# Kernel optimization log

Hardware: AMD Instinct MI355X
Metric: run time of the kernel (lower is better)

## Reference

```python
import jax, jax.numpy as jnp
import numpy as np
import math

B, L, H, E, D = 4, 2048, 8, 64, 64


def _build_local_log_symmetry_mask(L):
    # Faithful port of LocalLogSymmetryMask: True = masked-out position.
    lws = math.ceil(np.log2(L) / 2)  # local window size
    n_log = math.ceil(10 * np.log2(L))
    m = np.zeros((L, L), dtype=np.float32)
    for i in range(L):
        row = m[i]
        # left side: local window + log-spaced long-range
        if i - lws + 1 < 0:
            row[:i] = 1
        else:
            row[i - lws + 1:i + 1] = 1
            for k in range(n_log):
                ni = i - lws + 1 - int(1.5 ** k)
                if ni >= 0:
                    row[ni] = 1
                else:
                    break
        # right side (symmetric)
        if i + lws - 1 >= L:
            row[i:] = 1
        else:
            row[i:i + lws] = 1
            for k in range(n_log):
                ni = i + lws - 1 + int(1.5 ** k)
                if ni < L:
                    row[ni] = 1
                else:
                    break
    return m == 0  # True where attention is NOT allowed


def setup_inputs() -> dict:
    key = jax.random.key(0)
    kq, kk, kv = jax.random.split(key, 3)
    queries = jax.random.normal(kq, (B, L, H, E), dtype=jnp.float32)
    keys = jax.random.normal(kk, (B, L, H, E), dtype=jnp.float32)
    values = jax.random.normal(kv, (B, L, H, D), dtype=jnp.float32)
    mask = jnp.asarray(_build_local_log_symmetry_mask(L))  # [L, L] bool
    return {"queries": queries, "keys": keys, "values": values, "mask": mask}


def reference(queries, keys, values, mask):
    # queries/keys: [B,L,H,E], values: [B,L,H,D], mask: [L,L] bool (True = masked)
    E_ = queries.shape[-1]
    scale = 1.0 / math.sqrt(E_)
    # scores: [B,H,L,S]
    scores = jnp.einsum("blhe,bshe->bhls", queries, keys) * scale
    scores = jnp.where(mask[None, None, :, :], -jnp.inf, scores)
    attn = jax.nn.softmax(scores, axis=-1)  # dropout disabled (eval mode)
    out = jnp.einsum("bhls,bshd->blhd", attn, values)  # [B,L,H,D]
    return out
```

## Files before the change

### kernel.cpp

```cpp
#include <hip/hip_runtime.h>


#define KB 4
#define KL 2048
#define KH 8
#define KE 64
#define KWAVES 4
#define KROWS (KB * KL * KH)
#define KBLOCKS (KROWS / KWAVES)
#define KROWB (KH * KE * 4)
#define KVROWB 256
#define KWSBYTES ((size_t)KROWS * KVROWB)

typedef __fp16 h2 __attribute__((ext_vector_type(2)));
typedef unsigned ui4 __attribute__((ext_vector_type(4)));

static constexpr int kOff[48] = {
    -5, -4, -3, -2, -1, 0, 1, 2, 3, 4, 5,
    -6, -7, -8, -10, -12, -16, -22, -30, -43, -62, -91, -134, -199, -296,
    -442, -661, -990, -1482,
    6, 7, 8, 10, 12, 16, 22, 30, 43, 62, 91, 134, 199, 296, 442, 661, 990,
    1482,
    1 << 19};

template <int CTRL>
__device__ __forceinline__ float dpp_radd(float x) {
    int t = __builtin_amdgcn_update_dpp(0, __float_as_int(x), CTRL, 0xF, 0xF,
                                        false);
    return x + __int_as_float(t);
}
template <int CTRL>
__device__ __forceinline__ unsigned dpp_mov_u(unsigned x) {
    return (unsigned)__builtin_amdgcn_update_dpp(0, (int)x, CTRL, 0xF, 0xF,
                                                 false);
}

#if __has_builtin(__builtin_amdgcn_permlane16_swap)
__device__ __forceinline__ void pl16(float x, float& a, float& b) {
    auto r = __builtin_amdgcn_permlane16_swap(__float_as_uint(x),
                                              __float_as_uint(x), false, false);
    a = __uint_as_float(r[0]);
    b = __uint_as_float(r[1]);
}
#else
__device__ __forceinline__ void pl16(float x, float& a, float& b) {
    a = x;
    b = __shfl_xor(x, 16, 64);
}
#endif
#if __has_builtin(__builtin_amdgcn_permlane32_swap)
__device__ __forceinline__ void pl32(float x, float& a, float& b) {
    auto r = __builtin_amdgcn_permlane32_swap(__float_as_uint(x),
                                              __float_as_uint(x), false, false);
    a = __uint_as_float(r[0]);
    b = __uint_as_float(r[1]);
}
#else
__device__ __forceinline__ void pl32(float x, float& a, float& b) {
    a = x;
    b = __shfl_xor(x, 32, 64);
}
#endif
__device__ __forceinline__ float red16_add(float x) {
    float a, b;
    pl16(x, a, b);
    return a + b;
}
__device__ __forceinline__ float red32_add(float x) {
    float a, b;
    pl32(x, a, b);
    return a + b;
}

#if __has_builtin(__builtin_amdgcn_exp2f)
#define KEXP2(x) __builtin_amdgcn_exp2f(x)
#else
#define KEXP2(x) exp2f(x)
#endif

__device__ __forceinline__ h2 pkrtz(float a, float b) {
#if __has_builtin(__builtin_amdgcn_cvt_pkrtz)
    return __builtin_amdgcn_cvt_pkrtz(a, b);
#else
    h2 r;
    r[0] = (__fp16)a;
    r[1] = (__fp16)b;
    return r;
#endif
}
__device__ __forceinline__ float fd2(h2 a, h2 b, float c) {
#if __has_builtin(__builtin_amdgcn_fdot2)
    return __builtin_amdgcn_fdot2(a, b, c, false);
#else
    return fmaf((float)a[1], (float)b[1], fmaf((float)a[0], (float)b[0], c));
#endif
}
__device__ __forceinline__ h2 as_h2(unsigned u) {
    return __builtin_bit_cast(h2, u);
}

__global__ __launch_bounds__(256) void MaskAttention_prep_kernel(
    const float* __restrict__ k, const float* __restrict__ v,
    unsigned* __restrict__ kv) {
    const unsigned t  = (unsigned)blockIdx.x * 256u + (unsigned)threadIdx.x;
    const unsigned qd = t & 15u;
    const unsigned gr = t >> 4;
    const unsigned j  = gr & (KL - 1);
    const unsigned bh = gr >> 11;
    const unsigned b  = bh >> 3;
    const unsigned h  = bh & 7;
    const unsigned m  = qd >> 1;
    const float* __restrict__ src = (qd & 1u) ? v : k;
    const float* s =
        src + ((((size_t)b * KL + j) * KH + h) * KE + (size_t)m * 8);
    const float4 x = *(const float4*)s;
    const float4 y = *(const float4*)(s + 4);
    ui4 o;
    o[0] = __builtin_bit_cast(unsigned, pkrtz(x.x, x.y));
    o[1] = __builtin_bit_cast(unsigned, pkrtz(x.z, x.w));
    o[2] = __builtin_bit_cast(unsigned, pkrtz(y.x, y.y));
    o[3] = __builtin_bit_cast(unsigned, pkrtz(y.z, y.w));
    *(ui4*)((char*)kv + (size_t)gr * KVROWB + (size_t)qd * 16) = o;
}

__global__ __launch_bounds__(256) void MaskAttention_20572893347881_kernel(
    const float* __restrict__ q, const unsigned* __restrict__ kv,
    float* __restrict__ out) {
    const int tid  = (int)threadIdx.x;
    const int lane = tid & 63;
    const int g    = lane >> 4;
    const int e4   = lane & 15;
    const int wave = __builtin_amdgcn_readfirstlane(tid >> 6);

    const int p = (int)blockIdx.x;
    const int l = (p & 7) * (KBLOCKS / 8) + (p >> 3);
    const int r = l * KWAVES + wave;
    const int i  = r & (KL - 1);
    const int bh = r >> 11;

    const char* __restrict__ kvb =
        (const char*)kv + (size_t)bh * (KL * KVROWB);
    const size_t hbB = (size_t)(bh >> 3) * (KL * KROWB) +
                       (size_t)(bh & 7) * (KE * 4);
    const char* __restrict__ qc = (const char*)q + hbB;
    char* __restrict__ oc       = (char*)out + hbB;

    const unsigned co     = (unsigned)(e4 * 16);
    const unsigned base_r = (unsigned)i * KVROWB + co;
    const unsigned clampv = (unsigned)(KL - 1) * KVROWB + co;

    const bool g1 = (g & 1) != 0;
    const bool g2 = (g & 2) != 0;

    unsigned off[12];
    bool ok[12];
#pragma unroll
    for (int t = 0; t < 12; ++t) {
        const int a0 = kOff[4 * t + 0] * KVROWB;
        const int a1 = kOff[4 * t + 1] * KVROWB;
        const int a2 = kOff[4 * t + 2] * KVROWB;
        const int a3 = kOff[4 * t + 3] * KVROWB;
        const int dd = g1 ? (g2 ? a3 : a1) : (g2 ? a2 : a0);
        const unsigned u = base_r + (unsigned)dd;
        ok[t]  = u < (unsigned)(KL * KVROWB);
        off[t] = u < clampv ? u : clampv;
    }

    const float4 qf = *(const float4*)(qc + (unsigned)i * KROWB + co);
    const float qs  = 0.125f * 1.44269504088896340736f;
    const h2 qa = pkrtz(qf.x * qs, qf.y * qs);
    const h2 qb = pkrtz(qf.z * qs, qf.w * qs);
    const h2 qan =
        as_h2(dpp_mov_u<0x101>(__builtin_bit_cast(unsigned, qa)));
    const h2 qbn =
        as_h2(dpp_mov_u<0x101>(__builtin_bit_cast(unsigned, qb)));

    float dsum = 0.f;
    float a0 = 0.f, a1 = 0.f, a2 = 0.f, a3 = 0.f;
    float a4 = 0.f, a5 = 0.f, a6 = 0.f, a7 = 0.f;
#pragma unroll
    for (int t = 0; t < 12; ++t) {
        const ui4 w = *(const ui4*)(kvb + off[t]);
        float sd = fd2(as_h2(w[0]), qa,
                       fd2(as_h2(w[1]), qb,
                           fd2(as_h2(w[2]), qan, fd2(as_h2(w[3]), qbn, 0.f))));
        sd = dpp_radd<0x122>(sd);
        sd = dpp_radd<0x124>(sd);
        sd = dpp_radd<0x128>(sd);
        const float pp = ok[t] ? KEXP2(sd) : 0.f;
        const float pv =
            __uint_as_float(dpp_mov_u<0x111>(__float_as_uint(pp)));
        dsum += pv;
        const h2 v01 = as_h2(w[0]), v23 = as_h2(w[1]);
        const h2 v45 = as_h2(w[2]), v67 = as_h2(w[3]);
        a0 = fmaf(pv, (float)v01[0], a0);
        a1 = fmaf(pv, (float)v01[1], a1);
        a2 = fmaf(pv, (float)v23[0], a2);
        a3 = fmaf(pv, (float)v23[1], a3);
        a4 = fmaf(pv, (float)v45[0], a4);
        a5 = fmaf(pv, (float)v45[1], a5);
        a6 = fmaf(pv, (float)v67[0], a6);
        a7 = fmaf(pv, (float)v67[1], a7);
    }

    float d = red32_add(red16_add(dsum));
    const float inv = __builtin_amdgcn_rcpf(d);
    a0 = red32_add(red16_add(a0));
    a1 = red32_add(red16_add(a1));
    a2 = red32_add(red16_add(a2));
    a3 = red32_add(red16_add(a3));
    a4 = red32_add(red16_add(a4));
    a5 = red32_add(red16_add(a5));
    a6 = red32_add(red16_add(a6));
    a7 = red32_add(red16_add(a7));

    if ((lane < 16) && (lane & 1)) {
        const int m = lane >> 1;
        char* dst = oc + (unsigned)i * KROWB + (unsigned)m * 32;
        float4 o0 = make_float4(a0 * inv, a1 * inv, a2 * inv, a3 * inv);
        float4 o1 = make_float4(a4 * inv, a5 * inv, a6 * inv, a7 * inv);
        *(float4*)dst = o0;
        *(float4*)(dst + 16) = o1;
    }
}

__global__ __launch_bounds__(256) void MaskAttention_f32_fallback_kernel(
    const float* __restrict__ q, const float* __restrict__ k,
    const float* __restrict__ v, float* __restrict__ out) {
    const int tid  = (int)threadIdx.x;
    const int lane = tid & 63;
    const int g    = lane >> 4;
    const int e4   = lane & 15;
    const int wave = __builtin_amdgcn_readfirstlane(tid >> 6);
    const int p = (int)blockIdx.x;
    const int l = (p & 7) * (KBLOCKS / 8) + (p >> 3);
    const int r = l * KWAVES + wave;
    const int i = r & (KL - 1);
    const int h = (r >> 11) & (KH - 1);
    const int b = r >> 14;
    const size_t hbB = (size_t)b * (KL * KROWB) + (size_t)h * (KE * 4);
    const char* __restrict__ qc = (const char*)q + hbB;
    const char* __restrict__ kc = (const char*)k + hbB;
    const char* __restrict__ vc = (const char*)v + hbB;
    char* __restrict__ oc       = (char*)out + hbB;
    const unsigned co     = (unsigned)(e4 * 16);
    const unsigned base   = (unsigned)i * KROWB + co;
    const unsigned clampv = (unsigned)((KL - 1) * KROWB) + co;
    const bool g1 = (g & 1) != 0;
    const bool g2 = (g & 2) != 0;
    unsigned off[12];
    bool ok[12];
#pragma unroll
    for (int t = 0; t < 12; ++t) {
        const int a0 = kOff[4 * t + 0] * KROWB;
        const int a1 = kOff[4 * t + 1] * KROWB;
        const int a2 = kOff[4 * t + 2] * KROWB;
        const int a3 = kOff[4 * t + 3] * KROWB;
        const int dd = g1 ? (g2 ? a3 : a1) : (g2 ? a2 : a0);
        const unsigned u = base + (unsigned)dd;
        ok[t]  = u < (unsigned)(KL * KROWB);
        off[t] = u < clampv ? u : clampv;
    }
    float4 qf = *(const float4*)(qc + base);
    const float qs = 0.125f * 1.44269504088896340736f;
    qf.x *= qs; qf.y *= qs; qf.z *= qs; qf.w *= qs;
    float dsum = 0.f;
    float4 acc = make_float4(0.f, 0.f, 0.f, 0.f);
#pragma unroll
    for (int t = 0; t < 12; ++t) {
        const float4 kf = *(const float4*)(kc + off[t]);
        const float4 vf = *(const float4*)(vc + off[t]);
        float sd = qf.x * kf.x + qf.y * kf.y + qf.z * kf.z + qf.w * kf.w;
        sd = dpp_radd<0x121>(sd);
        sd = dpp_radd<0x122>(sd);
        sd = dpp_radd<0x124>(sd);
        sd = dpp_radd<0x128>(sd);
        const float pr = ok[t] ? KEXP2(sd) : 0.f;
        dsum += pr;
        acc.x = fmaf(pr, vf.x, acc.x);
        acc.y = fmaf(pr, vf.y, acc.y);
        acc.z = fmaf(pr, vf.z, acc.z);
        acc.w = fmaf(pr, vf.w, acc.w);
    }
    float d = red32_add(red16_add(dsum));
    const float inv = __builtin_amdgcn_rcpf(d);
    acc.x = red32_add(red16_add(acc.x));
    acc.y = red32_add(red16_add(acc.y));
    acc.z = red32_add(red16_add(acc.z));
    acc.w = red32_add(red16_add(acc.w));
    if (lane < 16) {
        float4 o = make_float4(acc.x * inv, acc.y * inv, acc.z * inv,
                               acc.w * inv);
        *(float4*)(oc + base) = o;
    }
}

extern "C" void kernel_launch(void* const* d_in, const int* in_sizes, int n_in,
                              void* d_out, int out_size, void* d_ws,
                              size_t ws_size, hipStream_t stream) {
    (void)in_sizes; (void)n_in; (void)out_size;
    const float* q = (const float*)d_in[0];
    const float* k = (const float*)d_in[1];
    const float* v = (const float*)d_in[2];
    float* out = (float*)d_out;

    if (d_ws != nullptr && ws_size >= KWSBYTES) {
        unsigned* kv = (unsigned*)d_ws;
        hipLaunchKernelGGL(MaskAttention_prep_kernel,
                           dim3(KROWS * 16 / 256), dim3(256), 0, stream,
                           k, v, kv);
        hipLaunchKernelGGL(MaskAttention_20572893347881_kernel,
                           dim3(KBLOCKS), dim3(KWAVES * 64), 0, stream,
                           q, kv, out);
    } else {
        hipLaunchKernelGGL(MaskAttention_f32_fallback_kernel,
                           dim3(KBLOCKS), dim3(KWAVES * 64), 0, stream,
                           q, k, v, out);
    }
}
```

Measured before the change: 142.9 us.

## Accumulate PV in packed fp16 FMA, table offsets in LDS, merge prep loads

Replaces the eight fp32 FMAs per key with four packed-half FMAs and does the cross-lane reductions on packed halves. Per-lane offset selection moves to a small LDS table, which adds a block barrier. The prep kernel now has each thread convert both the K and V slices, halving its grid, and the DPP move uses bound_ctrl. The aim is to cut ALU instruction count, at the risk of lower accumulation precision with fp16 sums.

```diff
diff --git a/kernel.cpp b/kernel.cpp
--- a/kernel.cpp
+++ b/kernel.cpp
@@ -30,46 +30,72 @@
     return x + __int_as_float(t);
 }
 template <int CTRL>
+__device__ __forceinline__ unsigned dpp_mov1_u(unsigned x) {
+#if __has_builtin(__builtin_amdgcn_mov_dpp)
+    return (unsigned)__builtin_amdgcn_mov_dpp((int)x, CTRL, 0xF, 0xF, true);
+#else
+    return (unsigned)__builtin_amdgcn_update_dpp(0, (int)x, CTRL, 0xF, 0xF,
+                                                 true);
+#endif
+}
+template <int CTRL>
 __device__ __forceinline__ unsigned dpp_mov_u(unsigned x) {
     return (unsigned)__builtin_amdgcn_update_dpp(0, (int)x, CTRL, 0xF, 0xF,
                                                  false);
 }
 
 #if __has_builtin(__builtin_amdgcn_permlane16_swap)
-__device__ __forceinline__ void pl16(float x, float& a, float& b) {
-    auto r = __builtin_amdgcn_permlane16_swap(__float_as_uint(x),
-                                              __float_as_uint(x), false, false);
-    a = __uint_as_float(r[0]);
-    b = __uint_as_float(r[1]);
-}
-#else
-__device__ __forceinline__ void pl16(float x, float& a, float& b) {
+#define KHAVE_PL16 1
+__device__ __forceinline__ void pl16u(unsigned x, unsigned& a, unsigned& b) {
+    auto r = __builtin_amdgcn_permlane16_swap(x, x, false, false);
+    a = r[0];
+    b = r[1];
+}
+#else
+#define KHAVE_PL16 0
+__device__ __forceinline__ void pl16u(unsigned x, unsigned& a, unsigned& b) {
     a = x;
-    b = __shfl_xor(x, 16, 64);
+    b = (unsigned)__shfl_xor((int)x, 16, 64);
 }
 #endif
 #if __has_builtin(__builtin_amdgcn_permlane32_swap)
-__device__ __forceinline__ void pl32(float x, float& a, float& b) {
-    auto r = __builtin_amdgcn_permlane32_swap(__float_as_uint(x),
-                                              __float_as_uint(x), false, false);
-    a = __uint_as_float(r[0]);
-    b = __uint_as_float(r[1]);
-}
-#else
-__device__ __forceinline__ void pl32(float x, float& a, float& b) {
+__device__ __forceinline__ void pl32u(unsigned x, unsigned& a, unsigned& b) {
+    auto r = __builtin_amdgcn_permlane32_swap(x, x, false, false);
+    a = r[0];
+    b = r[1];
+}
+#else
+__device__ __forceinline__ void pl32u(unsigned x, unsigned& a, unsigned& b) {
     a = x;
-    b = __shfl_xor(x, 32, 64);
-}
-#endif
+    b = (unsigned)__shfl_xor((int)x, 32, 64);
+}
+#endif
+
 __device__ __forceinline__ float red16_add(float x) {
-    float a, b;
-    pl16(x, a, b);
-    return a + b;
+    unsigned a, b;
+    pl16u(__float_as_uint(x), a, b);
+    return __uint_as_float(a) + __uint_as_float(b);
 }
 __device__ __forceinline__ float red32_add(float x) {
-    float a, b;
-    pl32(x, a, b);
-    return a + b;
+    unsigned a, b;
+    pl32u(__float_as_uint(x), a, b);
+    return __uint_as_float(a) + __uint_as_float(b);
+}
+__device__ __forceinline__ h2 as_h2(unsigned u) {
+    return __builtin_bit_cast(h2, u);
+}
+__device__ __forceinline__ unsigned as_u(h2 x) {
+    return __builtin_bit_cast(unsigned, x);
+}
+__device__ __forceinline__ h2 red16_pk(h2 x) {
+    unsigned a, b;
+    pl16u(as_u(x), a, b);
+    return as_h2(a) + as_h2(b);
+}
+__device__ __forceinline__ h2 red32_pk(h2 x) {
+    unsigned a, b;
+    pl32u(as_u(x), a, b);
+    return as_h2(a) + as_h2(b);
 }
 
 #if __has_builtin(__builtin_amdgcn_exp2f)
@@ -95,32 +121,36 @@
     return fmaf((float)a[1], (float)b[1], fmaf((float)a[0], (float)b[0], c));
 #endif
 }
-__device__ __forceinline__ h2 as_h2(unsigned u) {
-    return __builtin_bit_cast(h2, u);
-}
 
 __global__ __launch_bounds__(256) void MaskAttention_prep_kernel(
     const float* __restrict__ k, const float* __restrict__ v,
     unsigned* __restrict__ kv) {
     const unsigned t  = (unsigned)blockIdx.x * 256u + (unsigned)threadIdx.x;
-    const unsigned qd = t & 15u;
-    const unsigned gr = t >> 4;
+    const unsigned m  = t & 7u;
+    const unsigned gr = t >> 3;
     const unsigned j  = gr & (KL - 1);
     const unsigned bh = gr >> 11;
     const unsigned b  = bh >> 3;
     const unsigned h  = bh & 7;
-    const unsigned m  = qd >> 1;
-    const float* __restrict__ src = (qd & 1u) ? v : k;
-    const float* s =
-        src + ((((size_t)b * KL + j) * KH + h) * KE + (size_t)m * 8);
-    const float4 x = *(const float4*)s;
-    const float4 y = *(const float4*)(s + 4);
-    ui4 o;
-    o[0] = __builtin_bit_cast(unsigned, pkrtz(x.x, x.y));
-    o[1] = __builtin_bit_cast(unsigned, pkrtz(x.z, x.w));
-    o[2] = __builtin_bit_cast(unsigned, pkrtz(y.x, y.y));
-    o[3] = __builtin_bit_cast(unsigned, pkrtz(y.z, y.w));
-    *(ui4*)((char*)kv + (size_t)gr * KVROWB + (size_t)qd * 16) = o;
+    const size_t el = (((size_t)b * KL + j) * KH + h) * KE + (size_t)m * 8;
+    const float* sk = k + el;
+    const float* sv = v + el;
+    const float4 kx = *(const float4*)sk;
+    const float4 ky = *(const float4*)(sk + 4);
+    const float4 vx = *(const float4*)sv;
+    const float4 vy = *(const float4*)(sv + 4);
+    ui4 ok_, ov_;
+    ok_[0] = as_u(pkrtz(kx.x, kx.y));
+    ok_[1] = as_u(pkrtz(kx.z, kx.w));
+    ok_[2] = as_u(pkrtz(ky.x, ky.y));
+    ok_[3] = as_u(pkrtz(ky.z, ky.w));
+    ov_[0] = as_u(pkrtz(vx.x, vx.y));
+    ov_[1] = as_u(pkrtz(vx.z, vx.w));
+    ov_[2] = as_u(pkrtz(vy.x, vy.y));
+    ov_[3] = as_u(pkrtz(vy.z, vy.w));
+    char* dst = (char*)kv + (size_t)gr * KVROWB + (size_t)m * 32;
+    *(ui4*)dst        = ok_;
+    *(ui4*)(dst + 16) = ov_;
 }
 
 __global__ __launch_bounds__(256) void MaskAttention_20572893347881_kernel(
@@ -132,6 +162,10 @@
     const int e4   = lane & 15;
     const int wave = __builtin_amdgcn_readfirstlane(tid >> 6);
 
+    __shared__ int ddt[48];
+    if (tid < 48) ddt[tid] = kOff[tid] * KVROWB;
+    __syncthreads();
+
     const int p = (int)blockIdx.x;
     const int l = (p & 7) * (KBLOCKS / 8) + (p >> 3);
     const int r = l * KWAVES + wave;
@@ -149,19 +183,11 @@
     const unsigned base_r = (unsigned)i * KVROWB + co;
     const unsigned clampv = (unsigned)(KL - 1) * KVROWB + co;
 
-    const bool g1 = (g & 1) != 0;
-    const bool g2 = (g & 2) != 0;
-
     unsigned off[12];
     bool ok[12];
 #pragma unroll
     for (int t = 0; t < 12; ++t) {
-        const int a0 = kOff[4 * t + 0] * KVROWB;
-        const int a1 = kOff[4 * t + 1] * KVROWB;
-        const int a2 = kOff[4 * t + 2] * KVROWB;
-        const int a3 = kOff[4 * t + 3] * KVROWB;
-        const int dd = g1 ? (g2 ? a3 : a1) : (g2 ? a2 : a0);
-        const unsigned u = base_r + (unsigned)dd;
+        const unsigned u = base_r + (unsigned)ddt[4 * t + g];
         ok[t]  = u < (unsigned)(KL * KVROWB);
         off[t] = u < clampv ? u : clampv;
     }
@@ -170,14 +196,11 @@
     const float qs  = 0.125f * 1.44269504088896340736f;
     const h2 qa = pkrtz(qf.x * qs, qf.y * qs);
     const h2 qb = pkrtz(qf.z * qs, qf.w * qs);
-    const h2 qan =
-        as_h2(dpp_mov_u<0x101>(__builtin_bit_cast(unsigned, qa)));
-    const h2 qbn =
-        as_h2(dpp_mov_u<0x101>(__builtin_bit_cast(unsigned, qb)));
+    const h2 qan = as_h2(dpp_mov_u<0x101>(as_u(qa)));
+    const h2 qbn = as_h2(dpp_mov_u<0x101>(as_u(qb)));
 
     float dsum = 0.f;
-    float a0 = 0.f, a1 = 0.f, a2 = 0.f, a3 = 0.f;
-    float a4 = 0.f, a5 = 0.f, a6 = 0.f, a7 = 0.f;
+    h2 acc01 = {0, 0}, acc23 = {0, 0}, acc45 = {0, 0}, acc67 = {0, 0};
 #pragma unroll
     for (int t = 0; t < 12; ++t) {
         const ui4 w = *(const ui4*)(kvb + off[t]);
@@ -188,37 +211,29 @@
         sd = dpp_radd<0x124>(sd);
         sd = dpp_radd<0x128>(sd);
         const float pp = ok[t] ? KEXP2(sd) : 0.f;
-        const float pv =
-            __uint_as_float(dpp_mov_u<0x111>(__float_as_uint(pp)));
+        const float pv = __uint_as_float(dpp_mov1_u<0x111>(__float_as_uint(pp)));
         dsum += pv;
-        const h2 v01 = as_h2(w[0]), v23 = as_h2(w[1]);
-        const h2 v45 = as_h2(w[2]), v67 = as_h2(w[3]);
-        a0 = fmaf(pv, (float)v01[0], a0);
-        a1 = fmaf(pv, (float)v01[1], a1);
-        a2 = fmaf(pv, (float)v23[0], a2);
-        a3 = fmaf(pv, (float)v23[1], a3);
-        a4 = fmaf(pv, (float)v45[0], a4);
-        a5 = fmaf(pv, (float)v45[1], a5);
-        a6 = fmaf(pv, (float)v67[0], a6);
-        a7 = fmaf(pv, (float)v67[1], a7);
+        const h2 p2 = pkrtz(pv, pv);
+        acc01 = __builtin_elementwise_fma(p2, as_h2(w[0]), acc01);
+        acc23 = __builtin_elementwise_fma(p2, as_h2(w[1]), acc23);
+        acc45 = __builtin_elementwise_fma(p2, as_h2(w[2]), acc45);
+        acc67 = __builtin_elementwise_fma(p2, as_h2(w[3]), acc67);
     }
 
     float d = red32_add(red16_add(dsum));
     const float inv = __builtin_amdgcn_rcpf(d);
-    a0 = red32_add(red16_add(a0));
-    a1 = red32_add(red16_add(a1));
-    a2 = red32_add(red16_add(a2));
-    a3 = red32_add(red16_add(a3));
-    a4 = red32_add(red16_add(a4));
-    a5 = red32_add(red16_add(a5));
-    a6 = red32_add(red16_add(a6));
-    a7 = red32_add(red16_add(a7));
+    acc01 = red32_pk(red16_pk(acc01));
+    acc23 = red32_pk(red16_pk(acc23));
+    acc45 = red32_pk(red16_pk(acc45));
+    acc67 = red32_pk(red16_pk(acc67));
 
     if ((lane < 16) && (lane & 1)) {
         const int m = lane >> 1;
         char* dst = oc + (unsigned)i * KROWB + (unsigned)m * 32;
-        float4 o0 = make_float4(a0 * inv, a1 * inv, a2 * inv, a3 * inv);
-        float4 o1 = make_float4(a4 * inv, a5 * inv, a6 * inv, a7 * inv);
+        float4 o0 = make_float4((float)acc01[0] * inv, (float)acc01[1] * inv,
+                                (float)acc23[0] * inv, (float)acc23[1] * inv);
+        float4 o1 = make_float4((float)acc45[0] * inv, (float)acc45[1] * inv,
+                                (float)acc67[0] * inv, (float)acc67[1] * inv);
         *(float4*)dst = o0;
         *(float4*)(dst + 16) = o1;
     }
@@ -307,7 +322,7 @@
     if (d_ws != nullptr && ws_size >= KWSBYTES) {
         unsigned* kv = (unsigned*)d_ws;
         hipLaunchKernelGGL(MaskAttention_prep_kernel,
-                           dim3(KROWS * 16 / 256), dim3(256), 0, stream,
+                           dim3(KROWS * 8 / 256), dim3(256), 0, stream,
                            k, v, kv);
         hipLaunchKernelGGL(MaskAttention_20572893347881_kernel,
                            dim3(KBLOCKS), dim3(KWAVES * 64), 0, stream,
```

After: 139.2 us. 1.03x faster.
